# Kernel optimization log

Hardware: AMD Instinct MI355X
Metric: run time of the kernel (lower is better)

The kernel has to match this reference:

```python
import jax, jax.numpy as jnp
import numpy as np

EPS = 1e-5

def _layer_norm(x, w, b):
    mu = jnp.mean(x, axis=-1, keepdims=True)
    var = jnp.mean(jnp.square(x - mu), axis=-1, keepdims=True)
    return (x - mu) * jax.lax.rsqrt(var + EPS) * w + b

def setup_inputs() -> dict:
    key = jax.random.key(0)
    ks = jax.random.split(key, 8)
    B, S, D = 8, 2048, 1024
    image_features = jax.random.normal(ks[0], (B, S, D), dtype=jnp.float32)
    text_features = jax.random.normal(ks[1], (B, S, D), dtype=jnp.float32)
    ln_w = jnp.ones((D,), dtype=jnp.float32)
    ln_b = jnp.zeros((D,), dtype=jnp.float32)
    lim = 1.0 / np.sqrt(D)
    W_img = jax.random.uniform(ks[2], (D, D), minval=-lim, maxval=lim, dtype=jnp.float32)
    b_img = jax.random.uniform(ks[3], (D,), minval=-lim, maxval=lim, dtype=jnp.float32)
    W_txt = jax.random.uniform(ks[4], (D, D), minval=-lim, maxval=lim, dtype=jnp.float32)
    b_txt = jax.random.uniform(ks[5], (D,), minval=-lim, maxval=lim, dtype=jnp.float32)
    return {"image_features": image_features, "text_features": text_features,
            "ln_w": ln_w, "ln_b": ln_b, "W_img": W_img, "b_img": b_img,
            "W_txt": W_txt, "b_txt": b_txt}

def reference(image_features, text_features, ln_w, ln_b, W_img, b_img, W_txt, b_txt):
    D = image_features.shape[-1]
    scale = D ** (-0.5)
    image_norm = _layer_norm(image_features, ln_w, ln_b)
    text_norm = _layer_norm(text_features, ln_w, ln_b)
    # torch Linear: x @ W^T + b
    image_proj = jnp.einsum('bsd,ed->bse', image_norm, W_img) + b_img  # [B,Si,D]
    text_proj = jnp.einsum('btd,ed->bte', text_norm, W_txt) + b_txt    # [B,St,D]
    attn = jnp.einsum('bsd,btd->bst', image_proj, text_proj) * scale   # [B,Si,St]
    attn = jax.nn.softmax(attn, axis=-1)
    image_out = jnp.einsum('bst,btd->bsd', attn, text_proj)            # [B,Si,D]
    text_out = jnp.einsum('bst,bsd->btd', attn, image_proj)            # [B,St,D]
    return (image_out, text_out)
```

## Files before the change

### kernel.cpp

```cpp
#include <hip/hip_runtime.h>


#define DEV __device__ __forceinline__

typedef short s16x8 __attribute__((ext_vector_type(8)));
typedef float f32x4 __attribute__((ext_vector_type(4)));

DEV unsigned short f2bf(float f){
  unsigned u = __float_as_uint(f);
  u = (u + 0x7fffu + ((u >> 16) & 1u)) >> 16;
  return (unsigned short)u;
}
DEV float bf2f(unsigned short s){ return __uint_as_float(((unsigned)s) << 16); }

DEV void ldsload16(const void* g, void* l){
  __builtin_amdgcn_global_load_lds((const __attribute__((address_space(1))) void*)g,
                                   (__attribute__((address_space(3))) void*)l, 16, 0, 0);
}

__global__ __launch_bounds__(256) void k_cvt2(const float* __restrict__ sa,
                                              const float* __restrict__ sb,
                                              unsigned short* __restrict__ da,
                                              unsigned short* __restrict__ db, int n4){
  int i = blockIdx.x * 256 + threadIdx.x;
  const float* s; unsigned short* d; int j;
  if (i < n4){ s = sa; d = da; j = i; }
  else       { s = sb; d = db; j = i - n4; if (j >= n4) return; }
  float4 v = ((const float4*)s)[j];
  ushort4 o;
  o.x = f2bf(v.x); o.y = f2bf(v.y); o.z = f2bf(v.z); o.w = f2bf(v.w);
  ((ushort4*)d)[j] = o;
}

__global__ __launch_bounds__(256) void k_ln(const float* __restrict__ x,
                                            const float* __restrict__ w,
                                            const float* __restrict__ b,
                                            unsigned short* __restrict__ y){
  int row = blockIdx.x, tid = threadIdx.x;
  float4 v = ((const float4*)(x + (size_t)row * 1024))[tid];
  float s  = v.x + v.y + v.z + v.w;
  float s2 = v.x*v.x + v.y*v.y + v.z*v.z + v.w*v.w;
  #pragma unroll
  for (int o = 32; o > 0; o >>= 1){ s += __shfl_xor(s, o, 64); s2 += __shfl_xor(s2, o, 64); }
  __shared__ float sh[8];
  int wv = tid >> 6, ln = tid & 63;
  if (!ln){ sh[wv] = s; sh[4 + wv] = s2; }
  __syncthreads();
  s  = sh[0] + sh[1] + sh[2] + sh[3];
  s2 = sh[4] + sh[5] + sh[6] + sh[7];
  float mean = s * (1.f/1024.f);
  float var  = s2 * (1.f/1024.f) - mean * mean;
  float rstd = rsqrtf(var + 1e-5f);
  float4 w4 = ((const float4*)w)[tid];
  float4 b4 = ((const float4*)b)[tid];
  ushort4 o;
  o.x = f2bf((v.x-mean)*rstd*w4.x + b4.x);
  o.y = f2bf((v.y-mean)*rstd*w4.y + b4.y);
  o.z = f2bf((v.z-mean)*rstd*w4.z + b4.z);
  o.w = f2bf((v.w-mean)*rstd*w4.w + b4.w);
  ((ushort4*)(y + (size_t)row * 1024))[tid] = o;
}

#define STG(MAT, BASE, LD, T, H) do{                                              \
  ldsload16((BASE) + (size_t)(wave*16 + sfr) * (LD) + (T)*64 + (H)*32 + sq*8,     \
            &MAT[(T)&1][H][wave][0]);                                             \
  ldsload16((BASE) + (size_t)(wave*16 + 128 + sfr) * (LD) + (T)*64 + (H)*32 + sq*8,\
            &MAT[(T)&1][H][wave + 8][0]);                                         \
}while(0)

template<int OUT_BF16, int WRITE_T>
__global__ __launch_bounds__(512, 2) void k_gemm256(const unsigned short* __restrict__ A,
                                                    const unsigned short* __restrict__ Bt,
                                                    void* __restrict__ C,
                                                    unsigned short* __restrict__ ct,
                                                    const float* __restrict__ bias, float scale,
                                                    int K, int lda, int ldb, int ldc,
                                                    long sA, long sB, long sC,
                                                    int NBX, int NBY){
  __shared__ __align__(16) unsigned short SH[65536];
  typedef unsigned short (*Buf)[2][16][512];
  Buf As = (Buf)SH;
  Buf Bs = (Buf)(SH + 32768);
  int nwg = gridDim.x;
  int bid = blockIdx.x;
  int swz = (bid & 7) * (nwg >> 3) + (bid >> 3);
  int bx = swz % NBX; int rem = swz / NBX;
  int by = rem % NBY; int bz = rem / NBY;

  int tid = threadIdx.x, lane = tid & 63, wave = tid >> 6;
  int wm = wave >> 2, wn = wave & 3;
  int q = lane >> 4, fr = lane & 15;
  const unsigned short* Ab = A  + (size_t)bz * sA + (size_t)by * 256 * lda;
  const unsigned short* Bb = Bt + (size_t)bz * sB + (size_t)bx * 256 * ldb;
  int v   = (lane & 7) ^ ((lane >> 3) & 7);
  int sfr = 2 * (lane >> 3) + (v >> 2);
  int sq  = v & 3;
  int roff = ((fr >> 1) << 6) + (((q + ((fr & 1) << 2)) ^ ((fr >> 1) & 7)) << 3);
  int NT = K >> 6;

  f32x4 acc[8][4];
  #pragma unroll
  for (int m = 0; m < 8; ++m)
    #pragma unroll
    for (int n = 0; n < 4; ++n) acc[m][n] = f32x4{0.f, 0.f, 0.f, 0.f};

  STG(As, Ab, lda, 0, 0); STG(Bs, Bb, ldb, 0, 0);
  STG(As, Ab, lda, 0, 1); STG(Bs, Bb, ldb, 0, 1);
  STG(As, Ab, lda, 1, 0); STG(Bs, Bb, ldb, 1, 0);
  asm volatile("s_waitcnt vmcnt(8)");
  __builtin_amdgcn_s_barrier();

  for (int t = 0; t < NT; ++t){
    const int buf = t & 1;
    s16x8 bfr[4];
    #pragma unroll
    for (int ph = 0; ph < 4; ++ph){
      const int kk = ph >> 1;
      const unsigned short* Ah = &As[buf][kk][0][0];
      const unsigned short* Bh = &Bs[buf][kk][0][0];
      s16x8 af[4];
      if ((ph & 1) == 0){
        #pragma unroll
        for (int n = 0; n < 4; ++n)  bfr[n] = *(const s16x8*)&Bh[(wn*4 + n)*512 + roff];
        #pragma unroll
        for (int mi = 0; mi < 4; ++mi) af[mi] = *(const s16x8*)&Ah[(wm*8 + mi)*512 + roff];
      } else {
        #pragma unroll
        for (int mi = 0; mi < 4; ++mi) af[mi] = *(const s16x8*)&Ah[(wm*8 + 4 + mi)*512 + roff];
      }
      if (ph == 0){ if (t + 1 < NT) STG(As, Ab, lda, t + 1, 1); }
      if (ph == 1){ if (t + 1 < NT) STG(Bs, Bb, ldb, t + 1, 1); }
      if (ph == 2){ if (t + 2 < NT) STG(As, Ab, lda, t + 2, 0); }
      if (ph == 3){ if (t + 2 < NT) STG(Bs, Bb, ldb, t + 2, 0); }
      __builtin_amdgcn_s_barrier();
      asm volatile("s_waitcnt lgkmcnt(0)");
      __builtin_amdgcn_sched_barrier(0);
      __builtin_amdgcn_s_setprio(1);
      #pragma unroll
      for (int mi = 0; mi < 4; ++mi)
        #pragma unroll
        for (int n = 0; n < 4; ++n)
          acc[(ph&1)*4 + mi][n] = __builtin_amdgcn_mfma_f32_16x16x32_bf16(
              af[mi], bfr[n], acc[(ph&1)*4 + mi][n], 0, 0, 0);
      __builtin_amdgcn_s_setprio(0);
      __builtin_amdgcn_sched_barrier(0);
      if (ph & 1){
        if (t + 2 < NT) asm volatile("s_waitcnt vmcnt(8)");
        else            asm volatile("s_waitcnt vmcnt(0)");
      }
      __builtin_amdgcn_s_barrier();
    }
  }
  size_t cb = (size_t)bz * sC;
  int row0 = by*256 + wm*128 + q*4;
  int col0 = bx*256 + wn*64 + fr;
  #pragma unroll
  for (int m = 0; m < 8; ++m){
    #pragma unroll
    for (int n = 0; n < 4; ++n){
      int col = col0 + n*16;
      float bv = bias ? bias[col] : 0.f;
      #pragma unroll
      for (int j = 0; j < 4; ++j){
        int row = row0 + m*16 + j;
        float vv = acc[m][n][j] * scale + bv;
        if (OUT_BF16) ((unsigned short*)C)[cb + (size_t)row*ldc + col] = f2bf(vv);
        else          ((float*)C)[cb + (size_t)row*ldc + col] = vv;
      }
    }
  }
  if (WRITE_T){
    unsigned short* LT = SH;
    #pragma unroll
    for (int m = 0; m < 8; ++m){
      #pragma unroll
      for (int n = 0; n < 4; ++n){
        int tr = wn*64 + n*16 + fr;
        int tc = wm*128 + m*16 + q*4;
        float bv = bias ? bias[bx*256 + tr] : 0.f;
        ushort4 pk;
        pk.x = f2bf(acc[m][n][0] * scale + bv);
        pk.y = f2bf(acc[m][n][1] * scale + bv);
        pk.z = f2bf(acc[m][n][2] * scale + bv);
        pk.w = f2bf(acc[m][n][3] * scale + bv);
        int idx = tr*256 + (((tc >> 3) ^ (tr & 7)) << 3) + (tc & 7);
        *(ushort4*)&LT[idx] = pk;
      }
    }
    __syncthreads();
    int bb = by >> 3;
    int r2b = (by & 7) * 256;
    unsigned short* ctb = ct + (size_t)bb * 2097152 + r2b;
    #pragma unroll
    for (int p = 0; p < 16; ++p){
      int rr = p*16 + wave*2 + (lane >> 5);
      int ci = lane & 31;
      s16x8 rd = *(const s16x8*)&LT[rr*256 + ((ci ^ (rr & 7)) << 3)];
      *(s16x8*)&ctb[(size_t)(bx*256 + rr) * 2048 + ci*8] = rd;
    }
  }
}

__global__ __launch_bounds__(256) void k_transpose(const unsigned short* __restrict__ src,
                                                   unsigned short* __restrict__ dst,
                                                   int R, int C, long sS, long sD){
  __shared__ __align__(16) unsigned short tile[64 * 64];
  int tid = threadIdx.x;
  const unsigned short* sb = src + (size_t)blockIdx.z * sS;
  unsigned short* db = dst + (size_t)blockIdx.z * sD;
  int r0 = blockIdx.y * 64, c0 = blockIdx.x * 64;
  #pragma unroll
  for (int i = 0; i < 2; ++i){
    int ci = i * 256 + tid;
    int row = ci >> 3, cch = ci & 7;
    int pos = cch ^ (row & 7) ^ (row >> 3);
    uint4 v = *(const uint4*)&sb[(size_t)(r0 + row) * C + c0 + cch * 8];
    *(uint4*)&tile[row * 64 + pos * 8] = v;
  }
  __syncthreads();
  int ocp = tid >> 3, og = tid & 7;
  int oc = ocp * 2;
  union { uint4 v; unsigned short us[8]; } o0, o1;
  #pragma unroll
  for (int k = 0; k < 8; ++k){
    int r = og * 8 + k;
    int pos = (oc >> 3) ^ (r & 7) ^ (r >> 3);
    unsigned pr = *(const unsigned*)&tile[r * 64 + pos * 8 + (oc & 7)];
    o0.us[k] = (unsigned short)(pr & 0xffffu);
    o1.us[k] = (unsigned short)(pr >> 16);
  }
  *(uint4*)&db[(size_t)(c0 + oc    ) * R + r0 + og * 8] = o0.v;
  *(uint4*)&db[(size_t)(c0 + oc + 1) * R + r0 + og * 8] = o1.v;
}

__global__ __launch_bounds__(256) void k_softmax(unsigned short* __restrict__ a){
  size_t row = blockIdx.x;
  unsigned short* p = a + row * 2048;
  int tid = threadIdx.x;
  union { uint4 v; unsigned short us[8]; } in, out;
  in.v = *(const uint4*)&p[tid * 8];
  float x[8];
  #pragma unroll
  for (int j = 0; j < 8; ++j) x[j] = bf2f(in.us[j]);
  float mx = x[0];
  #pragma unroll
  for (int j = 1; j < 8; ++j) mx = fmaxf(mx, x[j]);
  #pragma unroll
  for (int o = 32; o > 0; o >>= 1) mx = fmaxf(mx, __shfl_xor(mx, o, 64));
  __shared__ float sh[8];
  int wv = tid >> 6, ln = tid & 63;
  if (!ln) sh[wv] = mx;
  __syncthreads();
  mx = fmaxf(fmaxf(sh[0], sh[1]), fmaxf(sh[2], sh[3]));
  float sm = 0.f, e[8];
  #pragma unroll
  for (int j = 0; j < 8; ++j){ e[j] = __expf(x[j] - mx); sm += e[j]; }
  #pragma unroll
  for (int o = 32; o > 0; o >>= 1) sm += __shfl_xor(sm, o, 64);
  if (!ln) sh[4 + wv] = sm;
  __syncthreads();
  sm = sh[4] + sh[5] + sh[6] + sh[7];
  float inv = 1.f / sm;
  #pragma unroll
  for (int j = 0; j < 8; ++j) out.us[j] = f2bf(e[j] * inv);
  *(uint4*)&p[tid * 8] = out.v;
}

extern "C" void kernel_launch(void* const* d_in, const int* in_sizes, int n_in,
                              void* d_out, int out_size, void* d_ws, size_t ws_size,
                              hipStream_t stream) {
  const float* img  = (const float*)d_in[0];
  const float* txt  = (const float*)d_in[1];
  const float* lnw  = (const float*)d_in[2];
  const float* lnb  = (const float*)d_in[3];
  const float* Wimg = (const float*)d_in[4];
  const float* bimg = (const float*)d_in[5];
  const float* Wtxt = (const float*)d_in[6];
  const float* btxt = (const float*)d_in[7];
  float* out = (float*)d_out;

  char* ws = (char*)d_ws;
  unsigned short* R1 = (unsigned short*)ws;
  unsigned short* R2 = (unsigned short*)(ws + 67108864);
  unsigned short* WB = (unsigned short*)(ws + 134217728);
  unsigned short* R4 = (unsigned short*)(ws + 138412032);

  const long PB = 2097152;
  const long AB = 4194304;

  k_cvt2<<<2048, 256, 0, stream>>>(Wimg, Wtxt, WB, WB + 1048576, 262144);
  k_ln<<<16384, 256, 0, stream>>>(img, lnw, lnb, R1);
  k_ln<<<16384, 256, 0, stream>>>(txt, lnw, lnb, R1 + 16777216);
  k_gemm256<1,1><<<256, 512, 0, stream>>>(R1,            WB,           R2,            R4,
                                          bimg, 1.f, 1024, 1024, 1024, 1024, 0, 0, 0, 4, 64);
  k_gemm256<1,1><<<256, 512, 0, stream>>>(R1 + 16777216, WB + 1048576, R2 + 16777216, R4 + 16777216,
                                          btxt, 1.f, 1024, 1024, 1024, 1024, 0, 0, 0, 4, 64);
  k_gemm256<1,0><<<512, 512, 0, stream>>>(R2, R2 + 16777216, R1, nullptr, nullptr, 0.03125f,
                                          1024, 1024, 1024, 2048, PB, PB, AB, 8, 8);
  k_softmax<<<16384, 256, 0, stream>>>(R1);
  dim3 gat(32, 32, 8);
  k_transpose<<<gat, 256, 0, stream>>>(R1, R2, 2048, 2048, AB, AB);
  k_gemm256<0,0><<<256, 512, 0, stream>>>(R1, R4 + 16777216, out, nullptr, nullptr, 1.f,
                                          2048, 2048, 2048, 1024, AB, PB, PB, 4, 8);
  k_gemm256<0,0><<<256, 512, 0, stream>>>(R2, R4, out + 16777216, nullptr, nullptr, 1.f,
                                          2048, 2048, 2048, 1024, AB, PB, PB, 4, 8);
}
```

Measured before the change: 406.8 us.

## Restructure GEMM main loop into two k-phases and merge layer-norm launches

The GEMM inner loop now runs two phases per tile, each loading all 8 A fragments and 4 B fragments and issuing 32 MFMAs, instead of four phases of 16 MFMAs. Both A and B prefetches are issued together, and the vmcnt waits are adjusted to match. This halves the barriers per k-tile at the cost of more live fragment registers. The two layer-norm launches are merged into one grid, and a syncthreads is added before the transposed LDS write so it cannot overwrite operand tiles still being read.

```diff
diff --git a/kernel.cpp b/kernel.cpp
--- a/kernel.cpp
+++ b/kernel.cpp
@@ -32,12 +32,16 @@
   ((ushort4*)d)[j] = o;
 }
 
-__global__ __launch_bounds__(256) void k_ln(const float* __restrict__ x,
-                                            const float* __restrict__ w,
-                                            const float* __restrict__ b,
-                                            unsigned short* __restrict__ y){
-  int row = blockIdx.x, tid = threadIdx.x;
-  float4 v = ((const float4*)(x + (size_t)row * 1024))[tid];
+__global__ __launch_bounds__(256) void k_ln2(const float* __restrict__ xa,
+                                             const float* __restrict__ xb,
+                                             const float* __restrict__ w,
+                                             const float* __restrict__ b,
+                                             unsigned short* __restrict__ ya,
+                                             unsigned short* __restrict__ yb){
+  int rb = blockIdx.x, tid = threadIdx.x;
+  const float* x; unsigned short* y;
+  if (rb < 16384){ x = xa; y = ya; } else { x = xb; y = yb; rb -= 16384; }
+  float4 v = ((const float4*)(x + (size_t)rb * 1024))[tid];
   float s  = v.x + v.y + v.z + v.w;
   float s2 = v.x*v.x + v.y*v.y + v.z*v.z + v.w*v.w;
   #pragma unroll
@@ -58,7 +62,7 @@
   o.y = f2bf((v.y-mean)*rstd*w4.y + b4.y);
   o.z = f2bf((v.z-mean)*rstd*w4.z + b4.z);
   o.w = f2bf((v.w-mean)*rstd*w4.w + b4.w);
-  ((ushort4*)(y + (size_t)row * 1024))[tid] = o;
+  ((ushort4*)(y + (size_t)rb * 1024))[tid] = o;
 }
 
 #define STG(MAT, BASE, LD, T, H) do{                                              \
@@ -112,41 +116,35 @@
 
   for (int t = 0; t < NT; ++t){
     const int buf = t & 1;
-    s16x8 bfr[4];
-    #pragma unroll
-    for (int ph = 0; ph < 4; ++ph){
-      const int kk = ph >> 1;
-      const unsigned short* Ah = &As[buf][kk][0][0];
-      const unsigned short* Bh = &Bs[buf][kk][0][0];
-      s16x8 af[4];
-      if ((ph & 1) == 0){
-        #pragma unroll
-        for (int n = 0; n < 4; ++n)  bfr[n] = *(const s16x8*)&Bh[(wn*4 + n)*512 + roff];
-        #pragma unroll
-        for (int mi = 0; mi < 4; ++mi) af[mi] = *(const s16x8*)&Ah[(wm*8 + mi)*512 + roff];
-      } else {
-        #pragma unroll
-        for (int mi = 0; mi < 4; ++mi) af[mi] = *(const s16x8*)&Ah[(wm*8 + 4 + mi)*512 + roff];
-      }
-      if (ph == 0){ if (t + 1 < NT) STG(As, Ab, lda, t + 1, 1); }
-      if (ph == 1){ if (t + 1 < NT) STG(Bs, Bb, ldb, t + 1, 1); }
-      if (ph == 2){ if (t + 2 < NT) STG(As, Ab, lda, t + 2, 0); }
-      if (ph == 3){ if (t + 2 < NT) STG(Bs, Bb, ldb, t + 2, 0); }
+    #pragma unroll
+    for (int ph = 0; ph < 2; ++ph){
+      const unsigned short* Ah = &As[buf][ph][0][0];
+      const unsigned short* Bh = &Bs[buf][ph][0][0];
+      s16x8 af[8], bfr[4];
+      #pragma unroll
+      for (int mi = 0; mi < 8; ++mi) af[mi] = *(const s16x8*)&Ah[(wm*8 + mi)*512 + roff];
+      #pragma unroll
+      for (int n = 0; n < 4; ++n)   bfr[n]  = *(const s16x8*)&Bh[(wn*4 + n)*512 + roff];
+      if (ph == 0){ if (t + 1 < NT){ STG(As, Ab, lda, t + 1, 1); STG(Bs, Bb, ldb, t + 1, 1); } }
+      else        { if (t + 2 < NT){ STG(As, Ab, lda, t + 2, 0); STG(Bs, Bb, ldb, t + 2, 0); } }
       __builtin_amdgcn_s_barrier();
       asm volatile("s_waitcnt lgkmcnt(0)");
       __builtin_amdgcn_sched_barrier(0);
       __builtin_amdgcn_s_setprio(1);
       #pragma unroll
-      for (int mi = 0; mi < 4; ++mi)
+      for (int mi = 0; mi < 8; ++mi)
         #pragma unroll
         for (int n = 0; n < 4; ++n)
-          acc[(ph&1)*4 + mi][n] = __builtin_amdgcn_mfma_f32_16x16x32_bf16(
-              af[mi], bfr[n], acc[(ph&1)*4 + mi][n], 0, 0, 0);
+          acc[mi][n] = __builtin_amdgcn_mfma_f32_16x16x32_bf16(af[mi], bfr[n], acc[mi][n], 0, 0, 0);
       __builtin_amdgcn_s_setprio(0);
       __builtin_amdgcn_sched_barrier(0);
-      if (ph & 1){
-        if (t + 2 < NT) asm volatile("s_waitcnt vmcnt(8)");
+      if (ph == 0){
+        if (t + 1 < NT) asm volatile("s_waitcnt vmcnt(8)");
         else            asm volatile("s_waitcnt vmcnt(0)");
+      } else {
+        if (t + 2 < NT)      asm volatile("s_waitcnt vmcnt(8)");
+        else if (t + 1 < NT) asm volatile("s_waitcnt vmcnt(4)");
+        else                 asm volatile("s_waitcnt vmcnt(0)");
       }
       __builtin_amdgcn_s_barrier();
     }
@@ -171,6 +169,7 @@
   }
   if (WRITE_T){
     unsigned short* LT = SH;
+    __syncthreads();
     #pragma unroll
     for (int m = 0; m < 8; ++m){
       #pragma unroll
@@ -289,8 +288,7 @@
   const long AB = 4194304;
 
   k_cvt2<<<2048, 256, 0, stream>>>(Wimg, Wtxt, WB, WB + 1048576, 262144);
-  k_ln<<<16384, 256, 0, stream>>>(img, lnw, lnb, R1);
-  k_ln<<<16384, 256, 0, stream>>>(txt, lnw, lnb, R1 + 16777216);
+  k_ln2<<<32768, 256, 0, stream>>>(img, txt, lnw, lnb, R1, R1 + 16777216);
   k_gemm256<1,1><<<256, 512, 0, stream>>>(R1,            WB,           R2,            R4,
                                           bimg, 1.f, 1024, 1024, 1024, 1024, 0, 0, 0, 4, 64);
   k_gemm256<1,1><<<256, 512, 0, stream>>>(R1 + 16777216, WB + 1048576, R2 + 16777216, R4 + 16777216,
```

New measurement: 410.6 us. About the same (+0.9%).

## Fuse softmax with transpose and merge the two layer-norm launches

Applied to the files above, without the earlier changes.

Replaces the separate row softmax and tiled transpose kernels with one kernel. It computes the row max and sum for 64 rows, then writes the normalized bf16 row in place and also writes its transpose through a swizzled LDS tile. This removes a full extra read of the attention matrix. The two layer-norm launches are merged into one grid, and a barrier is added before the GEMM reuses shared memory for its transposed output. The trade-off is that the fused kernel launches only 256 blocks, uses 4 threads per row and reads each row three times, which risks low occupancy and poorly coalesced, latency-bound access.

```diff
diff --git a/kernel.cpp b/kernel.cpp
--- a/kernel.cpp
+++ b/kernel.cpp
@@ -32,12 +32,16 @@
   ((ushort4*)d)[j] = o;
 }
 
-__global__ __launch_bounds__(256) void k_ln(const float* __restrict__ x,
-                                            const float* __restrict__ w,
-                                            const float* __restrict__ b,
-                                            unsigned short* __restrict__ y){
-  int row = blockIdx.x, tid = threadIdx.x;
-  float4 v = ((const float4*)(x + (size_t)row * 1024))[tid];
+__global__ __launch_bounds__(256) void k_ln2(const float* __restrict__ xa,
+                                             const float* __restrict__ xb,
+                                             const float* __restrict__ w,
+                                             const float* __restrict__ b,
+                                             unsigned short* __restrict__ ya,
+                                             unsigned short* __restrict__ yb){
+  int rb = blockIdx.x, tid = threadIdx.x;
+  const float* x; unsigned short* y;
+  if (rb < 16384){ x = xa; y = ya; } else { x = xb; y = yb; rb -= 16384; }
+  float4 v = ((const float4*)(x + (size_t)rb * 1024))[tid];
   float s  = v.x + v.y + v.z + v.w;
   float s2 = v.x*v.x + v.y*v.y + v.z*v.z + v.w*v.w;
   #pragma unroll
@@ -58,7 +62,7 @@
   o.y = f2bf((v.y-mean)*rstd*w4.y + b4.y);
   o.z = f2bf((v.z-mean)*rstd*w4.z + b4.z);
   o.w = f2bf((v.w-mean)*rstd*w4.w + b4.w);
-  ((ushort4*)(y + (size_t)row * 1024))[tid] = o;
+  ((ushort4*)(y + (size_t)rb * 1024))[tid] = o;
 }
 
 #define STG(MAT, BASE, LD, T, H) do{                                              \
@@ -171,6 +175,7 @@
   }
   if (WRITE_T){
     unsigned short* LT = SH;
+    __syncthreads();
     #pragma unroll
     for (int m = 0; m < 8; ++m){
       #pragma unroll
@@ -201,69 +206,62 @@
   }
 }
 
-__global__ __launch_bounds__(256) void k_transpose(const unsigned short* __restrict__ src,
-                                                   unsigned short* __restrict__ dst,
-                                                   int R, int C, long sS, long sD){
+__global__ __launch_bounds__(256) void k_softmax_t(unsigned short* __restrict__ a,
+                                                   unsigned short* __restrict__ at){
   __shared__ __align__(16) unsigned short tile[64 * 64];
   int tid = threadIdx.x;
-  const unsigned short* sb = src + (size_t)blockIdx.z * sS;
-  unsigned short* db = dst + (size_t)blockIdx.z * sD;
-  int r0 = blockIdx.y * 64, c0 = blockIdx.x * 64;
-  #pragma unroll
-  for (int i = 0; i < 2; ++i){
-    int ci = i * 256 + tid;
-    int row = ci >> 3, cch = ci & 7;
-    int pos = cch ^ (row & 7) ^ (row >> 3);
-    uint4 v = *(const uint4*)&sb[(size_t)(r0 + row) * C + c0 + cch * 8];
-    *(uint4*)&tile[row * 64 + pos * 8] = v;
-  }
-  __syncthreads();
-  int ocp = tid >> 3, og = tid & 7;
-  int oc = ocp * 2;
-  union { uint4 v; unsigned short us[8]; } o0, o1;
-  #pragma unroll
-  for (int k = 0; k < 8; ++k){
-    int r = og * 8 + k;
-    int pos = (oc >> 3) ^ (r & 7) ^ (r >> 3);
-    unsigned pr = *(const unsigned*)&tile[r * 64 + pos * 8 + (oc & 7)];
-    o0.us[k] = (unsigned short)(pr & 0xffffu);
-    o1.us[k] = (unsigned short)(pr >> 16);
-  }
-  *(uint4*)&db[(size_t)(c0 + oc    ) * R + r0 + og * 8] = o0.v;
-  *(uint4*)&db[(size_t)(c0 + oc + 1) * R + r0 + og * 8] = o1.v;
-}
-
-__global__ __launch_bounds__(256) void k_softmax(unsigned short* __restrict__ a){
-  size_t row = blockIdx.x;
-  unsigned short* p = a + row * 2048;
-  int tid = threadIdx.x;
-  union { uint4 v; unsigned short us[8]; } in, out;
-  in.v = *(const uint4*)&p[tid * 8];
-  float x[8];
-  #pragma unroll
-  for (int j = 0; j < 8; ++j) x[j] = bf2f(in.us[j]);
-  float mx = x[0];
-  #pragma unroll
-  for (int j = 1; j < 8; ++j) mx = fmaxf(mx, x[j]);
-  #pragma unroll
-  for (int o = 32; o > 0; o >>= 1) mx = fmaxf(mx, __shfl_xor(mx, o, 64));
-  __shared__ float sh[8];
-  int wv = tid >> 6, ln = tid & 63;
-  if (!ln) sh[wv] = mx;
-  __syncthreads();
-  mx = fmaxf(fmaxf(sh[0], sh[1]), fmaxf(sh[2], sh[3]));
-  float sm = 0.f, e[8];
-  #pragma unroll
-  for (int j = 0; j < 8; ++j){ e[j] = __expf(x[j] - mx); sm += e[j]; }
-  #pragma unroll
-  for (int o = 32; o > 0; o >>= 1) sm += __shfl_xor(sm, o, 64);
-  if (!ln) sh[4 + wv] = sm;
-  __syncthreads();
-  sm = sh[4] + sh[5] + sh[6] + sh[7];
-  float inv = 1.f / sm;
-  #pragma unroll
-  for (int j = 0; j < 8; ++j) out.us[j] = f2bf(e[j] * inv);
-  *(uint4*)&p[tid * 8] = out.v;
+  int r = tid >> 2, sub = tid & 3;
+  size_t boff = (size_t)blockIdx.y * 4194304;
+  int r0 = blockIdx.x * 64;
+  unsigned short* prow = a + boff + (size_t)(r0 + r) * 2048;
+  float mx = -3.0e38f;
+  for (int i = 0; i < 64; ++i){
+    union { uint4 v; unsigned short us[8]; } u;
+    u.v = *(const uint4*)&prow[(sub + 4*i) * 8];
+    #pragma unroll
+    for (int j = 0; j < 8; ++j) mx = fmaxf(mx, bf2f(u.us[j]));
+  }
+  mx = fmaxf(mx, __shfl_xor(mx, 1, 64));
+  mx = fmaxf(mx, __shfl_xor(mx, 2, 64));
+  float s = 0.f;
+  for (int i = 0; i < 64; ++i){
+    union { uint4 v; unsigned short us[8]; } u;
+    u.v = *(const uint4*)&prow[(sub + 4*i) * 8];
+    #pragma unroll
+    for (int j = 0; j < 8; ++j) s += __expf(bf2f(u.us[j]) - mx);
+  }
+  s += __shfl_xor(s, 1, 64);
+  s += __shfl_xor(s, 2, 64);
+  float inv = 1.f / s;
+  int ocp = tid >> 3, og = tid & 7, oc = ocp * 2;
+  for (int cb = 0; cb < 32; ++cb){
+    #pragma unroll
+    for (int jj = 0; jj < 2; ++jj){
+      int j = sub + jj*4;
+      int c8 = cb*8 + j;
+      union { uint4 v; unsigned short us[8]; } u, o;
+      u.v = *(const uint4*)&prow[c8 * 8];
+      #pragma unroll
+      for (int k = 0; k < 8; ++k) o.us[k] = f2bf(__expf(bf2f(u.us[k]) - mx) * inv);
+      *(uint4*)&prow[c8 * 8] = o.v;
+      int pos = j ^ (r & 7) ^ (r >> 3);
+      *(uint4*)&tile[r * 64 + pos * 8] = o.v;
+    }
+    __syncthreads();
+    union { uint4 v; unsigned short us[8]; } o0, o1;
+    #pragma unroll
+    for (int k = 0; k < 8; ++k){
+      int rr = og * 8 + k;
+      int pos = (oc >> 3) ^ (rr & 7) ^ (rr >> 3);
+      unsigned pr = *(const unsigned*)&tile[rr * 64 + pos * 8 + (oc & 7)];
+      o0.us[k] = (unsigned short)(pr & 0xffffu);
+      o1.us[k] = (unsigned short)(pr >> 16);
+    }
+    size_t c0 = (size_t)cb * 64;
+    *(uint4*)&at[boff + (c0 + oc    ) * 2048 + r0 + og * 8] = o0.v;
+    *(uint4*)&at[boff + (c0 + oc + 1) * 2048 + r0 + og * 8] = o1.v;
+    __syncthreads();
+  }
 }
 
 extern "C" void kernel_launch(void* const* d_in, const int* in_sizes, int n_in,
@@ -289,17 +287,15 @@
   const long AB = 4194304;
 
   k_cvt2<<<2048, 256, 0, stream>>>(Wimg, Wtxt, WB, WB + 1048576, 262144);
-  k_ln<<<16384, 256, 0, stream>>>(img, lnw, lnb, R1);
-  k_ln<<<16384, 256, 0, stream>>>(txt, lnw, lnb, R1 + 16777216);
+  k_ln2<<<32768, 256, 0, stream>>>(img, txt, lnw, lnb, R1, R1 + 16777216);
   k_gemm256<1,1><<<256, 512, 0, stream>>>(R1,            WB,           R2,            R4,
                                           bimg, 1.f, 1024, 1024, 1024, 1024, 0, 0, 0, 4, 64);
   k_gemm256<1,1><<<256, 512, 0, stream>>>(R1 + 16777216, WB + 1048576, R2 + 16777216, R4 + 16777216,
                                           btxt, 1.f, 1024, 1024, 1024, 1024, 0, 0, 0, 4, 64);
   k_gemm256<1,0><<<512, 512, 0, stream>>>(R2, R2 + 16777216, R1, nullptr, nullptr, 0.03125f,
                                           1024, 1024, 1024, 2048, PB, PB, AB, 8, 8);
-  k_softmax<<<16384, 256, 0, stream>>>(R1);
-  dim3 gat(32, 32, 8);
-  k_transpose<<<gat, 256, 0, stream>>>(R1, R2, 2048, 2048, AB, AB);
+  dim3 gs(32, 8);
+  k_softmax_t<<<gs, 256, 0, stream>>>(R1, R2);
   k_gemm256<0,0><<<256, 512, 0, stream>>>(R1, R4 + 16777216, out, nullptr, nullptr, 1.f,
                                           2048, 2048, 2048, 1024, AB, PB, PB, 4, 8);
   k_gemm256<0,0><<<256, 512, 0, stream>>>(R2, R4, out + 16777216, nullptr, nullptr, 1.f,
```

Measured after the change: 418.0 us. +2.8%, slower.
